# Performance work log

Hardware: AMD Instinct MI355X
Metric: run time of the kernel (lower is better)

## Reference

```python
import jax, jax.numpy as jnp
import numpy as np

R = 32      # voxel resolution (init kwarg)
EPS = 0.0   # init kwarg eps


def setup_inputs() -> dict:
    key = jax.random.key(0)
    k1, k2 = jax.random.split(key)
    features = jax.random.normal(k1, (8, 64, 100000), dtype=jnp.float32)
    coords = jax.random.normal(k2, (8, 3, 100000), dtype=jnp.float32)
    return {"features": features, "coords": coords}


def _voxelize(features, coords):
    # features: (B, C, N), coords: (B, 3, N)
    B, C, N = features.shape
    r = R
    # normalize coords to [0, 1] per batch (normalize=True branch)
    norm_coords = coords - coords.mean(axis=2, keepdims=True)
    norms = jnp.sqrt(jnp.sum(norm_coords * norm_coords, axis=1, keepdims=True))  # (B,1,N)
    scale = jnp.max(norms, axis=2, keepdims=True) * 2.0 + EPS                     # (B,1,1)
    norm_coords = norm_coords / scale + 0.5
    norm_coords = jnp.clip(norm_coords * r, 0.0, r - 1)                           # (B,3,N)
    vox = jnp.round(norm_coords).astype(jnp.int32)                                # (B,3,N)

    # flat voxel hash: b*r^3 + x*r^2 + y*r + z
    batch_id = jnp.arange(B, dtype=jnp.int32)[:, None]                            # (B,1)
    h = (batch_id * (r * r * r)
         + vox[:, 0, :] * (r * r)
         + vox[:, 1, :] * r
         + vox[:, 2, :]).reshape(-1)                                              # (B*N,)

    # one fused segment-sum over all channels (instead of per-channel scatter)
    feat_flat = features.transpose(0, 2, 1).reshape(B * N, C)                     # (B*N, C)
    num_seg = B * r * r * r
    sums = jax.ops.segment_sum(feat_flat, h, num_segments=num_seg)                # (B*r^3, C)
    counts = jax.ops.segment_sum(jnp.ones((B * N,), dtype=features.dtype), h,
                                 num_segments=num_seg)                            # (B*r^3,)
    counts = jnp.maximum(counts, 1.0)

    grid = (sums / counts[:, None]).reshape(B, r, r, r, C).transpose(0, 4, 1, 2, 3)
    return grid, norm_coords


def reference(features, coords):
    return _voxelize(features, coords)
```

## Files before the change

### kernel.cpp

```cpp
#include <hip/hip_runtime.h>

namespace {
constexpr int kB = 8;
constexpr int kC = 64;
constexpr int kN = 100000;
constexpr int kR = 32;
constexpr int kR3 = kR * kR * kR;
constexpr size_t kGridElems = (size_t)kB * kC * kR3;
constexpr int kNV = kB * kR3;
constexpr int kNQ = kNV / 4;
constexpr unsigned kTh = 32;
constexpr int kMaxHeavy = kB * kN / (int)(kTh + 1) + 2;

constexpr size_t kDsumOff = 0;
constexpr size_t kMaxOff = 192;
constexpr size_t kNlhOff = 240;
constexpr size_t kBsum3Off = 1024;
constexpr size_t kCountsOff = 8192;
constexpr size_t kOffsetsOff = kCountsOff + (size_t)kNV * 4;
constexpr size_t kLlistOff = kOffsetsOff + (size_t)(kNV + 64) * 4;
constexpr size_t kHlistOff = kLlistOff + (size_t)kNV * 4;
constexpr size_t kHashOff = kHlistOff + (size_t)kNQ * 4;
constexpr size_t kLrOff = kHashOff + (size_t)kB * kN * 2;
constexpr size_t kFeatTOff = kLrOff + (size_t)kB * kN * 4;
inline size_t wsNeed(int chunkB) { return kFeatTOff + (size_t)chunkB * kN * kC * 2; }
constexpr size_t kWsZeroBytes = kCountsOff + (size_t)kNV * 4;
constexpr unsigned kWsZeroBlks = (unsigned)(kWsZeroBytes / 16 / 256);
constexpr unsigned kOutZeroBlks = (unsigned)(kGridElems * 4 / 16 / 256);
}

__device__ __forceinline__ void f4add(float4& a, const float4& f) {
  a.x += f.x; a.y += f.y; a.z += f.z; a.w += f.w;
}
__device__ __forceinline__ unsigned short f2bf(float f) {
  const unsigned u = __float_as_uint(f);
  const unsigned rnd = 0x7FFFu + ((u >> 16) & 1u);
  return (unsigned short)((u + rnd) >> 16);
}
__device__ __forceinline__ float bf2f(unsigned short h) {
  return __uint_as_float((unsigned)h << 16);
}
__device__ __forceinline__ void bf4add(float4& a, const ushort4 f) {
  a.x += bf2f(f.x); a.y += bf2f(f.y); a.z += bf2f(f.z); a.w += bf2f(f.w);
}

__global__ __launch_bounds__(256) void zfill2_kernel(float4* __restrict__ out,
                                                     float4* __restrict__ ws) {
  const float4 z = make_float4(0.f, 0.f, 0.f, 0.f);
  const unsigned i = blockIdx.x;
  if (i < kOutZeroBlks)
    out[(size_t)i * 256 + threadIdx.x] = z;
  else
    ws[(size_t)(i - kOutZeroBlks) * 256 + threadIdx.x] = z;
}

__global__ __launch_bounds__(256) void mean_kernel(const float* __restrict__ coords,
                                                   double* __restrict__ dsum) {
  const int b = blockIdx.y;
  const int tid = blockIdx.x * blockDim.x + threadIdx.x;
  const int stride = gridDim.x * blockDim.x;
  const float* cb = coords + (size_t)b * 3 * kN;
  double s0 = 0.0, s1 = 0.0, s2 = 0.0;
  for (int n = tid; n < kN; n += stride) {
    s0 += (double)cb[n];
    s1 += (double)cb[kN + n];
    s2 += (double)cb[2 * kN + n];
  }
  __shared__ double sh[3][256];
  sh[0][threadIdx.x] = s0;
  sh[1][threadIdx.x] = s1;
  sh[2][threadIdx.x] = s2;
  __syncthreads();
  for (int off = 128; off > 0; off >>= 1) {
    if (threadIdx.x < (unsigned)off) {
      sh[0][threadIdx.x] += sh[0][threadIdx.x + off];
      sh[1][threadIdx.x] += sh[1][threadIdx.x + off];
      sh[2][threadIdx.x] += sh[2][threadIdx.x + off];
    }
    __syncthreads();
  }
  if (threadIdx.x == 0) {
    atomicAdd(&dsum[b * 3 + 0], sh[0][0]);
    atomicAdd(&dsum[b * 3 + 1], sh[1][0]);
    atomicAdd(&dsum[b * 3 + 2], sh[2][0]);
  }
}

__global__ __launch_bounds__(256) void maxnorm_kernel(const float* __restrict__ coords,
                                                      const double* __restrict__ dsum,
                                                      unsigned* __restrict__ maxbits) {
#pragma clang fp contract(off)
  const int b = blockIdx.y;
  const int tid = blockIdx.x * blockDim.x + threadIdx.x;
  const int stride = gridDim.x * blockDim.x;
  const float* cb = coords + (size_t)b * 3 * kN;
  const float m0 = (float)(dsum[b * 3 + 0] / (double)kN);
  const float m1 = (float)(dsum[b * 3 + 1] / (double)kN);
  const float m2 = (float)(dsum[b * 3 + 2] / (double)kN);
  float mx = 0.0f;
  for (int n = tid; n < kN; n += stride) {
    float x = cb[n] - m0;
    float y = cb[kN + n] - m1;
    float z = cb[2 * kN + n] - m2;
    float sx = x * x;
    float sy = y * y;
    float sz = z * z;
    float s = (sx + sy) + sz;
    mx = fmaxf(mx, s);
  }
  __shared__ float sh[256];
  sh[threadIdx.x] = mx;
  __syncthreads();
  for (int off = 128; off > 0; off >>= 1) {
    if (threadIdx.x < (unsigned)off)
      sh[threadIdx.x] = fmaxf(sh[threadIdx.x], sh[threadIdx.x + off]);
    __syncthreads();
  }
  if (threadIdx.x == 0) atomicMax(&maxbits[b], __float_as_uint(sh[0]));
}

__device__ __forceinline__ void point_geom(const float* __restrict__ coords,
                                           const double* __restrict__ dsum,
                                           const unsigned* __restrict__ maxbits,
                                           float* __restrict__ out_nc, int b, int n0,
                                           int h[4]) {
#pragma clang fp contract(off)
  const float m0 = (float)(dsum[b * 3 + 0] / (double)kN);
  const float m1 = (float)(dsum[b * 3 + 1] / (double)kN);
  const float m2 = (float)(dsum[b * 3 + 2] / (double)kN);
  const float scale = 2.0f * sqrtf(__uint_as_float(maxbits[b]));

  const float* cb = coords + (size_t)b * 3 * kN;
  const float4 cx = *(const float4*)(cb + n0);
  const float4 cy = *(const float4*)(cb + kN + n0);
  const float4 cz = *(const float4*)(cb + 2 * kN + n0);

  float xa[4] = {cx.x, cx.y, cx.z, cx.w};
  float ya[4] = {cy.x, cy.y, cy.z, cy.w};
  float za[4] = {cz.x, cz.y, cz.z, cz.w};
  float vx[4], vy[4], vz[4];
#pragma unroll
  for (int k = 0; k < 4; ++k) {
    float tx = (xa[k] - m0) / scale + 0.5f;
    float ty = (ya[k] - m1) / scale + 0.5f;
    float tz = (za[k] - m2) / scale + 0.5f;
    vx[k] = fminf(fmaxf(tx * 32.0f, 0.0f), 31.0f);
    vy[k] = fminf(fmaxf(ty * 32.0f, 0.0f), 31.0f);
    vz[k] = fminf(fmaxf(tz * 32.0f, 0.0f), 31.0f);
    int ix = (int)rintf(vx[k]);
    int iy = (int)rintf(vy[k]);
    int iz = (int)rintf(vz[k]);
    h[k] = ix * (kR * kR) + iy * kR + iz;
  }
  float* nb = out_nc + (size_t)b * 3 * kN;
  *(float4*)(nb + n0) = make_float4(vx[0], vx[1], vx[2], vx[3]);
  *(float4*)(nb + kN + n0) = make_float4(vy[0], vy[1], vy[2], vy[3]);
  *(float4*)(nb + 2 * kN + n0) = make_float4(vz[0], vz[1], vz[2], vz[3]);
}

__global__ __launch_bounds__(256) void hash_nc_kernel(
    const float* __restrict__ coords, const double* __restrict__ dsum,
    const unsigned* __restrict__ maxbits, float* __restrict__ out_nc,
    unsigned short* __restrict__ hashes, unsigned* __restrict__ lr,
    unsigned* __restrict__ counts) {
  const int b = blockIdx.y;
  const int n0 = (blockIdx.x * 256 + threadIdx.x) * 4;
  if (n0 >= kN) return;
  int h[4];
  point_geom(coords, dsum, maxbits, out_nc, b, n0, h);
  ushort4 h4;
  h4.x = (unsigned short)h[0];
  h4.y = (unsigned short)h[1];
  h4.z = (unsigned short)h[2];
  h4.w = (unsigned short)h[3];
  *(ushort4*)(hashes + (size_t)b * kN + n0) = h4;
  unsigned* cnt = counts + (size_t)b * kR3;
  uint4 l;
  l.x = atomicAdd(&cnt[h[0]], 1u);
  l.y = atomicAdd(&cnt[h[1]], 1u);
  l.z = atomicAdd(&cnt[h[2]], 1u);
  l.w = atomicAdd(&cnt[h[3]], 1u);
  *(uint4*)(lr + (size_t)b * kN + n0) = l;
}

__global__ __launch_bounds__(256) void scan_reduce(const unsigned* __restrict__ counts,
                                                   uint4* __restrict__ bsum3) {
  __shared__ unsigned sht[256], shl[256], shh[256];
  const int t = threadIdx.x;
  const uint4 c = ((const uint4*)counts)[blockIdx.x * 256 + t];
  const unsigned cnt[4] = {c.x, c.y, c.z, c.w};
  unsigned tot = 0, lt = 0, ht = 0;
#pragma unroll
  for (int k = 0; k < 4; ++k) {
    tot += cnt[k];
    lt += (cnt[k] >= 1u && cnt[k] <= kTh) ? 1u : 0u;
    ht += (cnt[k] > kTh) ? 1u : 0u;
  }
  sht[t] = tot;
  shl[t] = lt;
  shh[t] = ht;
  __syncthreads();
  for (int off = 128; off > 0; off >>= 1) {
    if (t < off) {
      sht[t] += sht[t + off];
      shl[t] += shl[t + off];
      shh[t] += shh[t + off];
    }
    __syncthreads();
  }
  if (t == 0) bsum3[blockIdx.x] = make_uint4(sht[0], shl[0], shh[0], 0u);
}

__global__ __launch_bounds__(256) void scan_bsum(uint4* __restrict__ bsum3) {
  __shared__ unsigned sht[256], shl[256], shh[256];
  const int t = threadIdx.x;
  const uint4 v = bsum3[t];
  sht[t] = v.x;
  shl[t] = v.y;
  shh[t] = v.z;
  __syncthreads();
  for (int d = 1; d < 256; d <<= 1) {
    const unsigned xt = (t >= d) ? sht[t - d] : 0u;
    const unsigned xl = (t >= d) ? shl[t - d] : 0u;
    const unsigned xh = (t >= d) ? shh[t - d] : 0u;
    __syncthreads();
    sht[t] += xt;
    shl[t] += xl;
    shh[t] += xh;
    __syncthreads();
  }
  bsum3[t] = make_uint4(sht[t] - v.x, shl[t] - v.y, shh[t] - v.z, 0u);
}

__global__ __launch_bounds__(256) void scan_write(const unsigned* __restrict__ counts,
                                                  const uint4* __restrict__ bsum3,
                                                  unsigned* __restrict__ offsets,
                                                  unsigned* __restrict__ Llist,
                                                  unsigned* __restrict__ Hlist,
                                                  unsigned* __restrict__ nlh) {
  __shared__ unsigned sht[256], shl[256], shh[256];
  const int t = threadIdx.x;
  const int gi = blockIdx.x * 256 + t;
  const int v0 = gi * 4;
  const uint4 c = ((const uint4*)counts)[gi];
  const unsigned cnt[4] = {c.x, c.y, c.z, c.w};
  unsigned lf[4], hf[4], tot = 0, lt = 0, ht = 0;
#pragma unroll
  for (int k = 0; k < 4; ++k) {
    lf[k] = (cnt[k] >= 1u && cnt[k] <= kTh) ? 1u : 0u;
    hf[k] = (cnt[k] > kTh) ? 1u : 0u;
    tot += cnt[k];
    lt += lf[k];
    ht += hf[k];
  }
  sht[t] = tot;
  shl[t] = lt;
  shh[t] = ht;
  __syncthreads();
  for (int d = 1; d < 256; d <<= 1) {
    const unsigned xt = (t >= d) ? sht[t - d] : 0u;
    const unsigned xl = (t >= d) ? shl[t - d] : 0u;
    const unsigned xh = (t >= d) ? shh[t - d] : 0u;
    __syncthreads();
    sht[t] += xt;
    shl[t] += xl;
    shh[t] += xh;
    __syncthreads();
  }
  const uint4 bs = bsum3[blockIdx.x];
  const unsigned base = bs.x + sht[t] - tot;
  uint4 o;
  o.x = base;
  o.y = o.x + cnt[0];
  o.z = o.y + cnt[1];
  o.w = o.z + cnt[2];
  ((uint4*)offsets)[gi] = o;
  if (gi == kNV / 4 - 1) offsets[kNV] = o.w + cnt[3];
  unsigned lbase = bs.y + shl[t] - lt;
  unsigned hbase = bs.z + shh[t] - ht;
#pragma unroll
  for (int k = 0; k < 4; ++k) {
    if (lf[k]) Llist[lbase++] = (unsigned)(v0 + k);
    if (hf[k]) Hlist[hbase++] = (unsigned)(v0 + k);
  }
  if (blockIdx.x == 255 && t == 255) {
    nlh[0] = lbase;
    nlh[1] = hbase;
  }
}

__global__ __launch_bounds__(256) void tr_kernel(const float* __restrict__ feat,
                                                 const unsigned short* __restrict__ hashes,
                                                 const unsigned* __restrict__ lr,
                                                 const unsigned* __restrict__ offsets,
                                                 unsigned short* __restrict__ feat_t,
                                                 int b0) {
  const int b2 = blockIdx.y;
  const int b = b0 + b2;
  const int n0 = blockIdx.x * 32;
  __shared__ float tile[64][33];
  __shared__ unsigned shr[32];
  if (threadIdx.x < 32) {
    const int n = n0 + threadIdx.x;
    const unsigned hh = hashes[(size_t)b * kN + n];
    const unsigned l = lr[(size_t)b * kN + n];
    shr[threadIdx.x] = offsets[(size_t)b * kR3 + hh] + l - (unsigned)b0 * (unsigned)kN;
  }
  const float* fb = feat + (size_t)b * kC * kN;
#pragma unroll
  for (int j = 0; j < 2; ++j) {
    const int idx = j * 256 + threadIdx.x;
    const int c = idx >> 3;
    const int q = idx & 7;
    const float4 v = *(const float4*)(fb + (size_t)c * kN + n0 + q * 4);
    tile[c][q * 4 + 0] = v.x;
    tile[c][q * 4 + 1] = v.y;
    tile[c][q * 4 + 2] = v.z;
    tile[c][q * 4 + 3] = v.w;
  }
  __syncthreads();
#pragma unroll
  for (int j = 0; j < 2; ++j) {
    const int idx = j * 256 + threadIdx.x;
    const int n = idx >> 4;
    const int cq = idx & 15;
    ushort4 w;
    w.x = f2bf(tile[cq * 4 + 0][n]);
    w.y = f2bf(tile[cq * 4 + 1][n]);
    w.z = f2bf(tile[cq * 4 + 2][n]);
    w.w = f2bf(tile[cq * 4 + 3][n]);
    const size_t row = (size_t)shr[n];
    *(ushort4*)(feat_t + row * kC + cq * 4) = w;
  }
}

__global__ __launch_bounds__(256) void gather_light(const unsigned short* __restrict__ feat_t,
                                                    const unsigned* __restrict__ offsets,
                                                    const unsigned* __restrict__ Llist,
                                                    const unsigned* __restrict__ nlh,
                                                    float* __restrict__ out, int b0,
                                                    int chunkB) {
  const unsigned nl = nlh[0];
  const int wid = blockIdx.x * 4 + (threadIdx.x >> 6);
  const int lane = threadIdx.x & 63;
  const int p = lane >> 4;
  const int cq = lane & 15;
  const unsigned i0 = (unsigned)wid * 4;
  if (i0 >= nl) return;
  const unsigned ip = i0 + (unsigned)p;
  bool act = ip < nl;
  const unsigned v = Llist[act ? ip : i0];
  const unsigned vlo = (unsigned)b0 * (unsigned)kR3;
  const unsigned vhi = (unsigned)(b0 + chunkB) * (unsigned)kR3;
  act = act && (v >= vlo) && (v < vhi);
  const unsigned s = offsets[v];
  unsigned e = offsets[v + 1];
  if (!act) e = s;
  const unsigned rb = (unsigned)b0 * (unsigned)kN;
  const unsigned short* ft = feat_t + cq * 4;
  float4 acc = make_float4(0.f, 0.f, 0.f, 0.f);
  unsigned r = s;
  for (; r + 2 <= e; r += 2) {
    const ushort4 f0 = *(const ushort4*)(ft + (size_t)(r - rb) * kC);
    const ushort4 f1 = *(const ushort4*)(ft + (size_t)(r + 1 - rb) * kC);
    bf4add(acc, f0);
    bf4add(acc, f1);
  }
  if (r < e) {
    const ushort4 f0 = *(const ushort4*)(ft + (size_t)(r - rb) * kC);
    bf4add(acc, f0);
  }
  if (act) {
    const float k = (float)(e - s);
    const int b = (int)(v >> 15);
    const int h = (int)(v & (kR3 - 1));
    float* ob = out + ((size_t)b * kC + cq * 4) * kR3 + h;
    ob[0] = acc.x / k;
    ob[(size_t)kR3] = acc.y / k;
    ob[(size_t)2 * kR3] = acc.z / k;
    ob[(size_t)3 * kR3] = acc.w / k;
  }
}

__global__ __launch_bounds__(256) void gather_heavy(const unsigned short* __restrict__ feat_t,
                                                    const unsigned* __restrict__ offsets,
                                                    const unsigned* __restrict__ Hlist,
                                                    const unsigned* __restrict__ nlh,
                                                    float* __restrict__ out, int b0,
                                                    int chunkB) {
  const unsigned nh = nlh[1];
  if (blockIdx.x >= nh) return;
  const unsigned v = Hlist[blockIdx.x];
  const unsigned vlo = (unsigned)b0 * (unsigned)kR3;
  const unsigned vhi = (unsigned)(b0 + chunkB) * (unsigned)kR3;
  if (v < vlo || v >= vhi) return;
  const unsigned s = offsets[v];
  const unsigned e = offsets[v + 1];
  const int slot = threadIdx.x >> 4;
  const int cq = threadIdx.x & 15;
  const unsigned rb = (unsigned)b0 * (unsigned)kN;
  float4 acc = make_float4(0.f, 0.f, 0.f, 0.f);
  for (unsigned r = s + (unsigned)slot; r < e; r += 16) {
    const ushort4 f = *(const ushort4*)(feat_t + (size_t)(r - rb) * kC + cq * 4);
    bf4add(acc, f);
  }
  __shared__ float sh[16][64];
  sh[slot][cq * 4 + 0] = acc.x;
  sh[slot][cq * 4 + 1] = acc.y;
  sh[slot][cq * 4 + 2] = acc.z;
  sh[slot][cq * 4 + 3] = acc.w;
  __syncthreads();
  if (threadIdx.x < 64) {
    const int c = threadIdx.x;
    float t = 0.f;
#pragma unroll
    for (int k = 0; k < 16; ++k) t += sh[k][c];
    const int b = (int)(v >> 15);
    const int h = (int)(v & (kR3 - 1));
    out[((size_t)b * kC + c) * kR3 + h] = t / (float)(e - s);
  }
}

__global__ __launch_bounds__(256) void scatter_direct(
    const float* __restrict__ feat, const float* __restrict__ coords,
    const double* __restrict__ dsum, const unsigned* __restrict__ maxbits,
    float* __restrict__ gridsum, float* __restrict__ out_nc,
    unsigned* __restrict__ counts) {
  const int b = blockIdx.y;
  const int n0 = (blockIdx.x * 256 + threadIdx.x) * 4;
  if (n0 >= kN) return;
  int h[4];
  point_geom(coords, dsum, maxbits, out_nc, b, n0, h);
  unsigned* cnt = counts + (size_t)b * kR3;
  atomicAdd(&cnt[h[0]], 1u);
  atomicAdd(&cnt[h[1]], 1u);
  atomicAdd(&cnt[h[2]], 1u);
  atomicAdd(&cnt[h[3]], 1u);
  const float* fb = feat + (size_t)b * kC * kN + n0;
  float* gb = gridsum + (size_t)b * kC * kR3;
#pragma unroll 8
  for (int c = 0; c < kC; ++c) {
    const float4 f = *(const float4*)(fb + (size_t)c * kN);
    float* g = gb + (size_t)c * kR3;
    unsafeAtomicAdd(g + h[0], f.x);
    unsafeAtomicAdd(g + h[1], f.y);
    unsafeAtomicAdd(g + h[2], f.z);
    unsafeAtomicAdd(g + h[3], f.w);
  }
}

__global__ __launch_bounds__(256) void divide_inplace(float* __restrict__ grid,
                                                      const unsigned* __restrict__ counts) {
  const size_t e = ((size_t)blockIdx.x * blockDim.x + threadIdx.x) * 4;
  if (e >= kGridElems) return;
  const int h = (int)(e & (size_t)(kR3 - 1));
  const int b = (int)(e >> 21);
  const uint4 cnt = *(const uint4*)(counts + (size_t)b * kR3 + h);
  float4 g = *(float4*)(grid + e);
  g.x = g.x / (float)(cnt.x > 1u ? cnt.x : 1u);
  g.y = g.y / (float)(cnt.y > 1u ? cnt.y : 1u);
  g.z = g.z / (float)(cnt.z > 1u ? cnt.z : 1u);
  g.w = g.w / (float)(cnt.w > 1u ? cnt.w : 1u);
  *(float4*)(grid + e) = g;
}

extern "C" void kernel_launch(void* const* d_in, const int* in_sizes, int n_in,
                              void* d_out, int out_size, void* d_ws, size_t ws_size,
                              hipStream_t stream) {
  const float* feat = (const float*)d_in[0];
  const float* coords = (const float*)d_in[1];
  float* out = (float*)d_out;
  float* out_nc = out + kGridElems;

  char* ws = (char*)d_ws;
  double* dsum = (double*)(ws + kDsumOff);
  unsigned* maxbits = (unsigned*)(ws + kMaxOff);
  unsigned* nlh = (unsigned*)(ws + kNlhOff);
  uint4* bsum3 = (uint4*)(ws + kBsum3Off);
  unsigned* counts = (unsigned*)(ws + kCountsOff);
  unsigned* offsets = (unsigned*)(ws + kOffsetsOff);
  unsigned* Llist = (unsigned*)(ws + kLlistOff);
  unsigned* Hlist = (unsigned*)(ws + kHlistOff);
  unsigned short* hashes = (unsigned short*)(ws + kHashOff);
  unsigned* lr = (unsigned*)(ws + kLrOff);
  unsigned short* feat_t = (unsigned short*)(ws + kFeatTOff);

  const dim3 blk(256);
  const int pblk = (kN / 4 + 255) / 256;

  int chunkB = 0;
  for (int c = kB; c >= 1; c >>= 1) {
    if (ws_size >= wsNeed(c)) { chunkB = c; break; }
  }

  if (chunkB) {
    zfill2_kernel<<<dim3(kOutZeroBlks + kWsZeroBlks), blk, 0, stream>>>((float4*)out,
                                                                        (float4*)ws);
    mean_kernel<<<dim3(32, kB), blk, 0, stream>>>(coords, dsum);
    maxnorm_kernel<<<dim3(32, kB), blk, 0, stream>>>(coords, dsum, maxbits);
    hash_nc_kernel<<<dim3(pblk, kB), blk, 0, stream>>>(coords, dsum, maxbits, out_nc,
                                                       hashes, lr, counts);
    scan_reduce<<<dim3(256), blk, 0, stream>>>(counts, bsum3);
    scan_bsum<<<dim3(1), blk, 0, stream>>>(bsum3);
    scan_write<<<dim3(256), blk, 0, stream>>>(counts, bsum3, offsets, Llist, Hlist, nlh);

    for (int b0 = 0; b0 < kB; b0 += chunkB) {
      tr_kernel<<<dim3(kN / 32, chunkB), blk, 0, stream>>>(feat, hashes, lr, offsets,
                                                           feat_t, b0);
      gather_light<<<dim3(kNV / 16), blk, 0, stream>>>(feat_t, offsets, Llist, nlh, out,
                                                       b0, chunkB);
      gather_heavy<<<dim3(kMaxHeavy), blk, 0, stream>>>(feat_t, offsets, Hlist, nlh, out,
                                                        b0, chunkB);
    }
  } else {
    zfill2_kernel<<<dim3(kOutZeroBlks + kWsZeroBlks), blk, 0, stream>>>((float4*)out,
                                                                        (float4*)ws);
    mean_kernel<<<dim3(32, kB), blk, 0, stream>>>(coords, dsum);
    maxnorm_kernel<<<dim3(32, kB), blk, 0, stream>>>(coords, dsum, maxbits);
    scatter_direct<<<dim3(pblk, kB), blk, 0, stream>>>(feat, coords, dsum, maxbits, out,
                                                       out_nc, counts);
    const size_t vec4 = kGridElems / 4;
    divide_inplace<<<dim3((unsigned)((vec4 + 255) / 256)), blk, 0, stream>>>(out, counts);
  }
}
```

Before: 194.5 us.

## Merge zero-fill with mean pass, fold block scan, fuse light/heavy gathers

Combines the zero-fill and coordinate-mean reduction into one launch, with the mean written as per-block partials instead of double atomics. The partials are finalized at the start of the maxnorm kernel, which also stores float means for later kernels. The separate block-sum scan kernel is removed: each scan_write block redoes the 256-entry prefix scan itself. The light and heavy gather kernels become one launch with block-index dispatch. The goal is fewer kernel launches and serial dependencies, at the cost of some redundant scan work per block.

```diff
diff --git a/kernel.cpp b/kernel.cpp
--- a/kernel.cpp
+++ b/kernel.cpp
@@ -11,12 +11,14 @@
 constexpr int kNQ = kNV / 4;
 constexpr unsigned kTh = 32;
 constexpr int kMaxHeavy = kB * kN / (int)(kTh + 1) + 2;
-
-constexpr size_t kDsumOff = 0;
-constexpr size_t kMaxOff = 192;
-constexpr size_t kNlhOff = 240;
-constexpr size_t kBsum3Off = 1024;
-constexpr size_t kCountsOff = 8192;
+constexpr int kLightBlks = kNV / 16;
+
+constexpr size_t kDpartOff = 0;
+constexpr size_t kMeanfOff = 6144;
+constexpr size_t kMaxOff = 6272;
+constexpr size_t kNlhOff = 6336;
+constexpr size_t kBsum3Off = 8192;
+constexpr size_t kCountsOff = 16384;
 constexpr size_t kOffsetsOff = kCountsOff + (size_t)kNV * 4;
 constexpr size_t kLlistOff = kOffsetsOff + (size_t)(kNV + 64) * 4;
 constexpr size_t kHlistOff = kLlistOff + (size_t)kNV * 4;
@@ -24,9 +26,10 @@
 constexpr size_t kLrOff = kHashOff + (size_t)kB * kN * 2;
 constexpr size_t kFeatTOff = kLrOff + (size_t)kB * kN * 4;
 inline size_t wsNeed(int chunkB) { return kFeatTOff + (size_t)chunkB * kN * kC * 2; }
-constexpr size_t kWsZeroBytes = kCountsOff + (size_t)kNV * 4;
-constexpr unsigned kWsZeroBlks = (unsigned)(kWsZeroBytes / 16 / 256);
+constexpr unsigned kMeanBlks = 256;
 constexpr unsigned kOutZeroBlks = (unsigned)(kGridElems * 4 / 16 / 256);
+constexpr unsigned kWsZeroF4 = (unsigned)((kCountsOff + (size_t)kNV * 4 - kMaxOff) / 16);
+constexpr unsigned kWsZeroBlks = (kWsZeroF4 + 255) / 256;
 }
 
 __device__ __forceinline__ void f4add(float4& a, const float4& f) {
@@ -44,59 +47,76 @@
   a.x += bf2f(f.x); a.y += bf2f(f.y); a.z += bf2f(f.z); a.w += bf2f(f.w);
 }
 
-__global__ __launch_bounds__(256) void zfill2_kernel(float4* __restrict__ out,
-                                                     float4* __restrict__ ws) {
-  const float4 z = make_float4(0.f, 0.f, 0.f, 0.f);
-  const unsigned i = blockIdx.x;
-  if (i < kOutZeroBlks)
-    out[(size_t)i * 256 + threadIdx.x] = z;
-  else
-    ws[(size_t)(i - kOutZeroBlks) * 256 + threadIdx.x] = z;
-}
-
-__global__ __launch_bounds__(256) void mean_kernel(const float* __restrict__ coords,
-                                                   double* __restrict__ dsum) {
-  const int b = blockIdx.y;
-  const int tid = blockIdx.x * blockDim.x + threadIdx.x;
-  const int stride = gridDim.x * blockDim.x;
-  const float* cb = coords + (size_t)b * 3 * kN;
-  double s0 = 0.0, s1 = 0.0, s2 = 0.0;
-  for (int n = tid; n < kN; n += stride) {
-    s0 += (double)cb[n];
-    s1 += (double)cb[kN + n];
-    s2 += (double)cb[2 * kN + n];
-  }
-  __shared__ double sh[3][256];
-  sh[0][threadIdx.x] = s0;
-  sh[1][threadIdx.x] = s1;
-  sh[2][threadIdx.x] = s2;
-  __syncthreads();
-  for (int off = 128; off > 0; off >>= 1) {
-    if (threadIdx.x < (unsigned)off) {
-      sh[0][threadIdx.x] += sh[0][threadIdx.x + off];
-      sh[1][threadIdx.x] += sh[1][threadIdx.x + off];
-      sh[2][threadIdx.x] += sh[2][threadIdx.x + off];
-    }
-    __syncthreads();
-  }
-  if (threadIdx.x == 0) {
-    atomicAdd(&dsum[b * 3 + 0], sh[0][0]);
-    atomicAdd(&dsum[b * 3 + 1], sh[1][0]);
-    atomicAdd(&dsum[b * 3 + 2], sh[2][0]);
+__global__ __launch_bounds__(256) void zm_kernel(const float* __restrict__ coords,
+                                                 double* __restrict__ dpart,
+                                                 float4* __restrict__ outz,
+                                                 float4* __restrict__ wsz) {
+  const unsigned bx = blockIdx.x;
+  if (bx < kMeanBlks) {
+    const int b = (int)(bx >> 5);
+    const int xb = (int)(bx & 31);
+    const float* cb = coords + (size_t)b * 3 * kN;
+    double s0 = 0.0, s1 = 0.0, s2 = 0.0;
+    for (int n = xb * 256 + (int)threadIdx.x; n < kN; n += 8192) {
+      s0 += (double)cb[n];
+      s1 += (double)cb[kN + n];
+      s2 += (double)cb[2 * kN + n];
+    }
+    __shared__ double sh[3][256];
+    sh[0][threadIdx.x] = s0;
+    sh[1][threadIdx.x] = s1;
+    sh[2][threadIdx.x] = s2;
+    __syncthreads();
+    for (int off = 128; off > 0; off >>= 1) {
+      if (threadIdx.x < (unsigned)off) {
+        sh[0][threadIdx.x] += sh[0][threadIdx.x + off];
+        sh[1][threadIdx.x] += sh[1][threadIdx.x + off];
+        sh[2][threadIdx.x] += sh[2][threadIdx.x + off];
+      }
+      __syncthreads();
+    }
+    if (threadIdx.x == 0) {
+      dpart[(size_t)bx * 3 + 0] = sh[0][0];
+      dpart[(size_t)bx * 3 + 1] = sh[1][0];
+      dpart[(size_t)bx * 3 + 2] = sh[2][0];
+    }
+  } else if (bx < kMeanBlks + kOutZeroBlks) {
+    outz[(size_t)(bx - kMeanBlks) * 256 + threadIdx.x] =
+        make_float4(0.f, 0.f, 0.f, 0.f);
+  } else {
+    const unsigned i = (bx - kMeanBlks - kOutZeroBlks) * 256 + threadIdx.x;
+    if (i < kWsZeroF4) wsz[i] = make_float4(0.f, 0.f, 0.f, 0.f);
   }
 }
 
 __global__ __launch_bounds__(256) void maxnorm_kernel(const float* __restrict__ coords,
-                                                      const double* __restrict__ dsum,
+                                                      const double* __restrict__ dpart,
+                                                      float* __restrict__ meanf,
                                                       unsigned* __restrict__ maxbits) {
 #pragma clang fp contract(off)
   const int b = blockIdx.y;
-  const int tid = blockIdx.x * blockDim.x + threadIdx.x;
-  const int stride = gridDim.x * blockDim.x;
+  __shared__ float m[3];
+  if (threadIdx.x == 0) {
+    double s0 = 0.0, s1 = 0.0, s2 = 0.0;
+    for (int j = 0; j < 32; ++j) {
+      s0 += dpart[(size_t)(b * 32 + j) * 3 + 0];
+      s1 += dpart[(size_t)(b * 32 + j) * 3 + 1];
+      s2 += dpart[(size_t)(b * 32 + j) * 3 + 2];
+    }
+    m[0] = (float)(s0 / (double)kN);
+    m[1] = (float)(s1 / (double)kN);
+    m[2] = (float)(s2 / (double)kN);
+    if (blockIdx.x == 0) {
+      meanf[b * 3 + 0] = m[0];
+      meanf[b * 3 + 1] = m[1];
+      meanf[b * 3 + 2] = m[2];
+    }
+  }
+  __syncthreads();
+  const float m0 = m[0], m1 = m[1], m2 = m[2];
+  const int tid = blockIdx.x * 256 + threadIdx.x;
+  const int stride = gridDim.x * 256;
   const float* cb = coords + (size_t)b * 3 * kN;
-  const float m0 = (float)(dsum[b * 3 + 0] / (double)kN);
-  const float m1 = (float)(dsum[b * 3 + 1] / (double)kN);
-  const float m2 = (float)(dsum[b * 3 + 2] / (double)kN);
   float mx = 0.0f;
   for (int n = tid; n < kN; n += stride) {
     float x = cb[n] - m0;
@@ -120,14 +140,14 @@
 }
 
 __device__ __forceinline__ void point_geom(const float* __restrict__ coords,
-                                           const double* __restrict__ dsum,
+                                           const float* __restrict__ meanf,
                                            const unsigned* __restrict__ maxbits,
                                            float* __restrict__ out_nc, int b, int n0,
                                            int h[4]) {
 #pragma clang fp contract(off)
-  const float m0 = (float)(dsum[b * 3 + 0] / (double)kN);
-  const float m1 = (float)(dsum[b * 3 + 1] / (double)kN);
-  const float m2 = (float)(dsum[b * 3 + 2] / (double)kN);
+  const float m0 = meanf[b * 3 + 0];
+  const float m1 = meanf[b * 3 + 1];
+  const float m2 = meanf[b * 3 + 2];
   const float scale = 2.0f * sqrtf(__uint_as_float(maxbits[b]));
 
   const float* cb = coords + (size_t)b * 3 * kN;
@@ -159,7 +179,7 @@
 }
 
 __global__ __launch_bounds__(256) void hash_nc_kernel(
-    const float* __restrict__ coords, const double* __restrict__ dsum,
+    const float* __restrict__ coords, const float* __restrict__ meanf,
     const unsigned* __restrict__ maxbits, float* __restrict__ out_nc,
     unsigned short* __restrict__ hashes, unsigned* __restrict__ lr,
     unsigned* __restrict__ counts) {
@@ -167,7 +187,7 @@
   const int n0 = (blockIdx.x * 256 + threadIdx.x) * 4;
   if (n0 >= kN) return;
   int h[4];
-  point_geom(coords, dsum, maxbits, out_nc, b, n0, h);
+  point_geom(coords, meanf, maxbits, out_nc, b, n0, h);
   ushort4 h4;
   h4.x = (unsigned short)h[0];
   h4.y = (unsigned short)h[1];
@@ -211,27 +231,6 @@
   if (t == 0) bsum3[blockIdx.x] = make_uint4(sht[0], shl[0], shh[0], 0u);
 }
 
-__global__ __launch_bounds__(256) void scan_bsum(uint4* __restrict__ bsum3) {
-  __shared__ unsigned sht[256], shl[256], shh[256];
-  const int t = threadIdx.x;
-  const uint4 v = bsum3[t];
-  sht[t] = v.x;
-  shl[t] = v.y;
-  shh[t] = v.z;
-  __syncthreads();
-  for (int d = 1; d < 256; d <<= 1) {
-    const unsigned xt = (t >= d) ? sht[t - d] : 0u;
-    const unsigned xl = (t >= d) ? shl[t - d] : 0u;
-    const unsigned xh = (t >= d) ? shh[t - d] : 0u;
-    __syncthreads();
-    sht[t] += xt;
-    shl[t] += xl;
-    shh[t] += xh;
-    __syncthreads();
-  }
-  bsum3[t] = make_uint4(sht[t] - v.x, shl[t] - v.y, shh[t] - v.z, 0u);
-}
-
 __global__ __launch_bounds__(256) void scan_write(const unsigned* __restrict__ counts,
                                                   const uint4* __restrict__ bsum3,
                                                   unsigned* __restrict__ offsets,
@@ -240,6 +239,25 @@
                                                   unsigned* __restrict__ nlh) {
   __shared__ unsigned sht[256], shl[256], shh[256];
   const int t = threadIdx.x;
+  const uint4 bv = bsum3[t];
+  sht[t] = bv.x;
+  shl[t] = bv.y;
+  shh[t] = bv.z;
+  __syncthreads();
+  for (int d = 1; d < 256; d <<= 1) {
+    const unsigned xt = (t >= d) ? sht[t - d] : 0u;
+    const unsigned xl = (t >= d) ? shl[t - d] : 0u;
+    const unsigned xh = (t >= d) ? shh[t - d] : 0u;
+    __syncthreads();
+    sht[t] += xt;
+    shl[t] += xl;
+    shh[t] += xh;
+    __syncthreads();
+  }
+  const unsigned bbt = (blockIdx.x > 0) ? sht[blockIdx.x - 1] : 0u;
+  const unsigned bbl = (blockIdx.x > 0) ? shl[blockIdx.x - 1] : 0u;
+  const unsigned bbh = (blockIdx.x > 0) ? shh[blockIdx.x - 1] : 0u;
+  __syncthreads();
   const int gi = blockIdx.x * 256 + t;
   const int v0 = gi * 4;
   const uint4 c = ((const uint4*)counts)[gi];
@@ -267,8 +285,7 @@
     shh[t] += xh;
     __syncthreads();
   }
-  const uint4 bs = bsum3[blockIdx.x];
-  const unsigned base = bs.x + sht[t] - tot;
+  const unsigned base = bbt + sht[t] - tot;
   uint4 o;
   o.x = base;
   o.y = o.x + cnt[0];
@@ -276,8 +293,8 @@
   o.w = o.z + cnt[2];
   ((uint4*)offsets)[gi] = o;
   if (gi == kNV / 4 - 1) offsets[kNV] = o.w + cnt[3];
-  unsigned lbase = bs.y + shl[t] - lt;
-  unsigned hbase = bs.z + shh[t] - ht;
+  unsigned lbase = bbl + shl[t] - lt;
+  unsigned hbase = bbh + shh[t] - ht;
 #pragma unroll
   for (int k = 0; k < 4; ++k) {
     if (lf[k]) Llist[lbase++] = (unsigned)(v0 + k);
@@ -334,103 +351,98 @@
   }
 }
 
-__global__ __launch_bounds__(256) void gather_light(const unsigned short* __restrict__ feat_t,
-                                                    const unsigned* __restrict__ offsets,
-                                                    const unsigned* __restrict__ Llist,
-                                                    const unsigned* __restrict__ nlh,
-                                                    float* __restrict__ out, int b0,
-                                                    int chunkB) {
-  const unsigned nl = nlh[0];
-  const int wid = blockIdx.x * 4 + (threadIdx.x >> 6);
-  const int lane = threadIdx.x & 63;
-  const int p = lane >> 4;
-  const int cq = lane & 15;
-  const unsigned i0 = (unsigned)wid * 4;
-  if (i0 >= nl) return;
-  const unsigned ip = i0 + (unsigned)p;
-  bool act = ip < nl;
-  const unsigned v = Llist[act ? ip : i0];
+__global__ __launch_bounds__(256) void gather_kernel(const unsigned short* __restrict__ feat_t,
+                                                     const unsigned* __restrict__ offsets,
+                                                     const unsigned* __restrict__ Llist,
+                                                     const unsigned* __restrict__ Hlist,
+                                                     const unsigned* __restrict__ nlh,
+                                                     float* __restrict__ out, int b0,
+                                                     int chunkB) {
+  const unsigned rb = (unsigned)b0 * (unsigned)kN;
   const unsigned vlo = (unsigned)b0 * (unsigned)kR3;
   const unsigned vhi = (unsigned)(b0 + chunkB) * (unsigned)kR3;
-  act = act && (v >= vlo) && (v < vhi);
-  const unsigned s = offsets[v];
-  unsigned e = offsets[v + 1];
-  if (!act) e = s;
-  const unsigned rb = (unsigned)b0 * (unsigned)kN;
-  const unsigned short* ft = feat_t + cq * 4;
-  float4 acc = make_float4(0.f, 0.f, 0.f, 0.f);
-  unsigned r = s;
-  for (; r + 2 <= e; r += 2) {
-    const ushort4 f0 = *(const ushort4*)(ft + (size_t)(r - rb) * kC);
-    const ushort4 f1 = *(const ushort4*)(ft + (size_t)(r + 1 - rb) * kC);
-    bf4add(acc, f0);
-    bf4add(acc, f1);
-  }
-  if (r < e) {
-    const ushort4 f0 = *(const ushort4*)(ft + (size_t)(r - rb) * kC);
-    bf4add(acc, f0);
-  }
-  if (act) {
-    const float k = (float)(e - s);
-    const int b = (int)(v >> 15);
-    const int h = (int)(v & (kR3 - 1));
-    float* ob = out + ((size_t)b * kC + cq * 4) * kR3 + h;
-    ob[0] = acc.x / k;
-    ob[(size_t)kR3] = acc.y / k;
-    ob[(size_t)2 * kR3] = acc.z / k;
-    ob[(size_t)3 * kR3] = acc.w / k;
-  }
-}
-
-__global__ __launch_bounds__(256) void gather_heavy(const unsigned short* __restrict__ feat_t,
-                                                    const unsigned* __restrict__ offsets,
-                                                    const unsigned* __restrict__ Hlist,
-                                                    const unsigned* __restrict__ nlh,
-                                                    float* __restrict__ out, int b0,
-                                                    int chunkB) {
-  const unsigned nh = nlh[1];
-  if (blockIdx.x >= nh) return;
-  const unsigned v = Hlist[blockIdx.x];
-  const unsigned vlo = (unsigned)b0 * (unsigned)kR3;
-  const unsigned vhi = (unsigned)(b0 + chunkB) * (unsigned)kR3;
-  if (v < vlo || v >= vhi) return;
-  const unsigned s = offsets[v];
-  const unsigned e = offsets[v + 1];
-  const int slot = threadIdx.x >> 4;
-  const int cq = threadIdx.x & 15;
-  const unsigned rb = (unsigned)b0 * (unsigned)kN;
-  float4 acc = make_float4(0.f, 0.f, 0.f, 0.f);
-  for (unsigned r = s + (unsigned)slot; r < e; r += 16) {
-    const ushort4 f = *(const ushort4*)(feat_t + (size_t)(r - rb) * kC + cq * 4);
-    bf4add(acc, f);
-  }
-  __shared__ float sh[16][64];
-  sh[slot][cq * 4 + 0] = acc.x;
-  sh[slot][cq * 4 + 1] = acc.y;
-  sh[slot][cq * 4 + 2] = acc.z;
-  sh[slot][cq * 4 + 3] = acc.w;
-  __syncthreads();
-  if (threadIdx.x < 64) {
-    const int c = threadIdx.x;
-    float t = 0.f;
-#pragma unroll
-    for (int k = 0; k < 16; ++k) t += sh[k][c];
-    const int b = (int)(v >> 15);
-    const int h = (int)(v & (kR3 - 1));
-    out[((size_t)b * kC + c) * kR3 + h] = t / (float)(e - s);
+
+  if (blockIdx.x < (unsigned)kLightBlks) {
+    const unsigned nl = nlh[0];
+    const int wid = blockIdx.x * 4 + (threadIdx.x >> 6);
+    const int lane = threadIdx.x & 63;
+    const int p = lane >> 4;
+    const int cq = lane & 15;
+    const unsigned i0 = (unsigned)wid * 4;
+    if (i0 >= nl) return;
+    const unsigned ip = i0 + (unsigned)p;
+    bool act = ip < nl;
+    const unsigned v = Llist[act ? ip : i0];
+    act = act && (v >= vlo) && (v < vhi);
+    const unsigned s = offsets[v];
+    unsigned e = offsets[v + 1];
+    if (!act) e = s;
+    const unsigned short* ft = feat_t + cq * 4;
+    float4 acc = make_float4(0.f, 0.f, 0.f, 0.f);
+    unsigned r = s;
+    for (; r + 2 <= e; r += 2) {
+      const ushort4 f0 = *(const ushort4*)(ft + (size_t)(r - rb) * kC);
+      const ushort4 f1 = *(const ushort4*)(ft + (size_t)(r + 1 - rb) * kC);
+      bf4add(acc, f0);
+      bf4add(acc, f1);
+    }
+    if (r < e) {
+      const ushort4 f0 = *(const ushort4*)(ft + (size_t)(r - rb) * kC);
+      bf4add(acc, f0);
+    }
+    if (act) {
+      const float k = (float)(e - s);
+      const int b = (int)(v >> 15);
+      const int h = (int)(v & (kR3 - 1));
+      float* ob = out + ((size_t)b * kC + cq * 4) * kR3 + h;
+      ob[0] = acc.x / k;
+      ob[(size_t)kR3] = acc.y / k;
+      ob[(size_t)2 * kR3] = acc.z / k;
+      ob[(size_t)3 * kR3] = acc.w / k;
+    }
+  } else {
+    const unsigned hb = blockIdx.x - (unsigned)kLightBlks;
+    const unsigned nh = nlh[1];
+    if (hb >= nh) return;
+    const unsigned v = Hlist[hb];
+    if (v < vlo || v >= vhi) return;
+    const unsigned s = offsets[v];
+    const unsigned e = offsets[v + 1];
+    const int slot = threadIdx.x >> 4;
+    const int cq = threadIdx.x & 15;
+    float4 acc = make_float4(0.f, 0.f, 0.f, 0.f);
+    for (unsigned r = s + (unsigned)slot; r < e; r += 16) {
+      const ushort4 f = *(const ushort4*)(feat_t + (size_t)(r - rb) * kC + cq * 4);
+      bf4add(acc, f);
+    }
+    __shared__ float sh[16][64];
+    sh[slot][cq * 4 + 0] = acc.x;
+    sh[slot][cq * 4 + 1] = acc.y;
+    sh[slot][cq * 4 + 2] = acc.z;
+    sh[slot][cq * 4 + 3] = acc.w;
+    __syncthreads();
+    if (threadIdx.x < 64) {
+      const int c = threadIdx.x;
+      float t = 0.f;
+#pragma unroll
+      for (int k = 0; k < 16; ++k) t += sh[k][c];
+      const int b = (int)(v >> 15);
+      const int h = (int)(v & (kR3 - 1));
+      out[((size_t)b * kC + c) * kR3 + h] = t / (float)(e - s);
+    }
   }
 }
 
 __global__ __launch_bounds__(256) void scatter_direct(
     const float* __restrict__ feat, const float* __restrict__ coords,
-    const double* __restrict__ dsum, const unsigned* __restrict__ maxbits,
+    const float* __restrict__ meanf, const unsigned* __restrict__ maxbits,
     float* __restrict__ gridsum, float* __restrict__ out_nc,
     unsigned* __restrict__ counts) {
   const int b = blockIdx.y;
   const int n0 = (blockIdx.x * 256 + threadIdx.x) * 4;
   if (n0 >= kN) return;
   int h[4];
-  point_geom(coords, dsum, maxbits, out_nc, b, n0, h);
+  point_geom(coords, meanf, maxbits, out_nc, b, n0, h);
   unsigned* cnt = counts + (size_t)b * kR3;
   atomicAdd(&cnt[h[0]], 1u);
   atomicAdd(&cnt[h[1]], 1u);
@@ -473,7 +485,8 @@
   float* out_nc = out + kGridElems;
 
   char* ws = (char*)d_ws;
-  double* dsum = (double*)(ws + kDsumOff);
+  double* dpart = (double*)(ws + kDpartOff);
+  float* meanf = (float*)(ws + kMeanfOff);
   unsigned* maxbits = (unsigned*)(ws + kMaxOff);
   unsigned* nlh = (unsigned*)(ws + kNlhOff);
   uint4* bsum3 = (uint4*)(ws + kBsum3Off);
@@ -493,31 +506,24 @@
     if (ws_size >= wsNeed(c)) { chunkB = c; break; }
   }
 
+  zm_kernel<<<dim3(kMeanBlks + kOutZeroBlks + kWsZeroBlks), blk, 0, stream>>>(
+      coords, dpart, (float4*)out, (float4*)(ws + kMaxOff));
+  maxnorm_kernel<<<dim3(32, kB), blk, 0, stream>>>(coords, dpart, meanf, maxbits);
+
   if (chunkB) {
-    zfill2_kernel<<<dim3(kOutZeroBlks + kWsZeroBlks), blk, 0, stream>>>((float4*)out,
-                                                                        (float4*)ws);
-    mean_kernel<<<dim3(32, kB), blk, 0, stream>>>(coords, dsum);
-    maxnorm_kernel<<<dim3(32, kB), blk, 0, stream>>>(coords, dsum, maxbits);
-    hash_nc_kernel<<<dim3(pblk, kB), blk, 0, stream>>>(coords, dsum, maxbits, out_nc,
+    hash_nc_kernel<<<dim3(pblk, kB), blk, 0, stream>>>(coords, meanf, maxbits, out_nc,
                                                        hashes, lr, counts);
     scan_reduce<<<dim3(256), blk, 0, stream>>>(counts, bsum3);
-    scan_bsum<<<dim3(1), blk, 0, stream>>>(bsum3);
     scan_write<<<dim3(256), blk, 0, stream>>>(counts, bsum3, offsets, Llist, Hlist, nlh);
 
     for (int b0 = 0; b0 < kB; b0 += chunkB) {
       tr_kernel<<<dim3(kN / 32, chunkB), blk, 0, stream>>>(feat, hashes, lr, offsets,
                                                            feat_t, b0);
-      gather_light<<<dim3(kNV / 16), blk, 0, stream>>>(feat_t, offsets, Llist, nlh, out,
-                                                       b0, chunkB);
-      gather_heavy<<<dim3(kMaxHeavy), blk, 0, stream>>>(feat_t, offsets, Hlist, nlh, out,
-                                                        b0, chunkB);
+      gather_kernel<<<dim3(kLightBlks + kMaxHeavy), blk, 0, stream>>>(
+          feat_t, offsets, Llist, Hlist, nlh, out, b0, chunkB);
     }
   } else {
-    zfill2_kernel<<<dim3(kOutZeroBlks + kWsZeroBlks), blk, 0, stream>>>((float4*)out,
-                                                                        (float4*)ws);
-    mean_kernel<<<dim3(32, kB), blk, 0, stream>>>(coords, dsum);
-    maxnorm_kernel<<<dim3(32, kB), blk, 0, stream>>>(coords, dsum, maxbits);
-    scatter_direct<<<dim3(pblk, kB), blk, 0, stream>>>(feat, coords, dsum, maxbits, out,
+    scatter_direct<<<dim3(pblk, kB), blk, 0, stream>>>(feat, coords, meanf, maxbits, out,
                                                        out_nc, counts);
     const size_t vec4 = kGridElems / 4;
     divide_inplace<<<dim3((unsigned)((vec4 + 255) / 256)), blk, 0, stream>>>(out, counts);
```

Result: faster. 179.9 us (-7.5%).
